# Kernel optimization log

Measured on AMD Instinct MI355X. Metric: run time of the kernel, lower is better.

## Reference

```python
import jax, jax.numpy as jnp
import numpy as np

jax.config.update("jax_enable_x64", True)

_FULL = 1 << 32
_MASK = _FULL - 1
_HALF = _FULL >> 1
_QUARTER = _HALF >> 1
_THREE_QUARTER = 3 * _QUARTER


def setup_inputs() -> dict:
    key = jax.random.key(0)
    num_symbols = 262144            # e.g. a 512x512 plane of {-1,+1} symbols
    num_bits = 2 * num_symbols      # compressed payload, ~2 bits/symbol budget
    payload_bits = jax.random.randint(key, (num_bits,), 0, 2, dtype=jnp.int64)
    return {
        "payload_bits": payload_bits,
        "total_freq": 4096,         # 1 << frequency_precision (12)
        "num_symbols": num_symbols,
        "context_bits": 8,
    }


def reference(payload_bits, total_freq, num_symbols, context_bits):
    bits = payload_bits.astype(jnp.int64)
    nb = bits.shape[0]
    num_states = 1 << context_bits
    smask = num_states - 1

    def read_bit(ptr):
        # _BitReader returns 0 past the end of the payload
        return jnp.where(ptr < nb, bits[jnp.clip(ptr, 0, nb - 1)], jnp.int64(0))

    # initial 32-bit code word
    idx32 = jnp.arange(32, dtype=jnp.int64)
    b32 = jnp.where(idx32 < nb, bits[jnp.clip(idx32, 0, nb - 1)], 0)
    code0 = jnp.sum(b32 << (31 - idx32))

    def renorm(carry):
        # E1/E2/E3 renormalization loop (bit-level, data dependent)
        def cond(c):
            low, high, code, ptr = c
            return (high < _HALF) | (low >= _HALF) | ((low >= _QUARTER) & (high < _THREE_QUARTER))

        def body(c):
            low, high, code, ptr = c
            sub = jnp.where(high < _HALF, jnp.int64(0),
                            jnp.where(low >= _HALF, jnp.int64(_HALF), jnp.int64(_QUARTER)))
            low = low - sub
            high = high - sub
            code = code - sub
            low = (low << 1) & _MASK
            high = ((high << 1) & _MASK) | 1
            code = ((code << 1) & _MASK) | read_bit(ptr)
            return (low, high, code, ptr + 1)

        return jax.lax.while_loop(cond, body, carry)

    def step(carry, _):
        low, high, code, ptr, state, count0, count1 = carry
        n0 = count0[state]
        n1 = count1[state]
        total = n0 + n1
        p0 = n0.astype(jnp.float64) / total.astype(jnp.float64)
        p0_freq = jnp.clip(jnp.rint(p0 * (total_freq - 2)) + 1.0, 1.0, float(total_freq - 1)).astype(jnp.int64)
        rng = high - low + 1                      # fits int64 (<= 2^32)
        scaled = ((code - low + 1) * total_freq - 1) // rng
        split = low + rng * p0_freq // total_freq
        bit = (scaled >= p0_freq).astype(jnp.int64)
        low2 = jnp.where(bit == 0, low, split)
        high2 = jnp.where(bit == 0, split - 1, high)
        low3, high3, code3, ptr3 = renorm((low2, high2, code, ptr))
        count0 = count0.at[state].add(1 - bit)
        count1 = count1.at[state].add(bit)
        state2 = ((state << 1) | bit) & smask
        return (low3, high3, code3, ptr3, state2, count0, count1), bit

    init = (
        jnp.int64(0),               # low
        jnp.int64(_MASK),           # high = 2^32 - 1
        code0.astype(jnp.int64),    # code
        jnp.int64(32),              # bit pointer (32 bits consumed)
        jnp.int64(0),               # context state
        jnp.ones(num_states, dtype=jnp.int64),  # count0 (Laplace init)
        jnp.ones(num_states, dtype=jnp.int64),  # count1
    )
    _, out_bits = jax.lax.scan(step, init, None, length=num_symbols)
    # map {0,1} -> {-1,+1} float32 symbols (reshape to bitstream.shape is metadata-only)
    return out_bits.astype(jnp.float32) * 2.0 - 1.0
```

## Files before the change

kernel.cpp:

```cpp
#include <hip/hip_runtime.h>


#define WORDS_LDS 16400
#define MAX_STATES 1024
#define OBITS_WORDS 8192

__device__ __forceinline__ long long ddiv_floor(long long n, long long d) {
    double qd = (double)n / (double)d;
    long long q = (long long)qd;
    long long r = n - q * d;
    q -= (r < 0);
    q += (r >= d);
    return q;
}

__device__ __forceinline__ void decode_fast(
    const unsigned* __restrict__ words, unsigned* tab, unsigned* obits,
    unsigned total_freq, int tf_shift, int num_symbols, int smask, unsigned pf0)
{
    const unsigned H = 0x80000000u;
    unsigned low = 0u, high = 0xFFFFFFFFu;
    unsigned dlt = words[0];
    unsigned long long bitbuf = (((unsigned long long)words[1]) << 32)
                              | (unsigned long long)words[2];
    int unavail = 64;
    unsigned pre = words[3];
    int widx = 4;
    unsigned wnext = words[4];

    const unsigned tfm2_2 = (total_freq - 2u) << 1;
    const double tfm2d = (double)(total_freq - 2u);
    const int tfm1 = (int)(total_freq - 1u);

    int st = 0, stP = -1;
    unsigned entN0 = 1u, entPK = 1u | (pf0 << 20);
    unsigned P0n0 = 1u, P0pk = entPK;
    unsigned P1n0 = 1u, P1pk = entPK;
    unsigned uN0p = 0u, uPKp = 0u;

    const int iters = num_symbols >> 5;
    for (int it = 0; it < iters; ++it) {
        unsigned obuf = 0u;
        #pragma unroll
        for (int u = 0; u < 32; ++u) {
            const int gbase = ((st << 2) & smask) * 2;
            const uint4 Ga = *reinterpret_cast<const uint4*>(tab + gbase);
            const uint4 Gb = *reinterpret_cast<const uint4*>(tab + gbase + 4);

            const unsigned pf  = entPK >> 20;
            const unsigned n1v = entPK & 0xFFFFFu;
            const unsigned n0v = entN0;
            const unsigned rngm1 = high - low;
            const unsigned long long P = (unsigned long long)pf * rngm1 + pf;
            const unsigned soff = (unsigned)(P >> tf_shift);
            const bool bt = (dlt >= soff);
            const unsigned bitv = bt ? 1u : 0u;
            const unsigned split = low + soff;
            low  = bt ? split : low;
            high = bt ? high : (split - 1u);
            dlt  = bt ? (dlt - soff) : dlt;
            obuf = (obuf << 1) | bitv;

            const unsigned nn0 = n0v + 1u - bitv;
            const unsigned nn1 = n1v + bitv;
            const unsigned tt  = nn0 + nn1;
            const unsigned d2  = tt << 1;
            const unsigned num2 = __umul24(tfm2_2, nn0) + tt;
            const float qf = (float)num2 * __builtin_amdgcn_rcpf((float)d2);
            unsigned qi = (unsigned)qf;
            int r = (int)(num2 - __umul24(qi, d2));
            if (r < 0)        { qi -= 1u; r += (int)d2; }
            if (r >= (int)d2) { qi += 1u; r -= (int)d2; }
            unsigned pfn = qi + 1u;
            if (__builtin_expect(__builtin_amdgcn_readfirstlane(r) == 0, 0)) {
                asm volatile("");
                double p0d = (double)(int)nn0 / (double)(int)tt;
                double pfd = rint(p0d * tfm2d) + 1.0;
                int pfi = (int)pfd;
                pfi = pfi < 1 ? 1 : (pfi > tfm1 ? tfm1 : pfi);
                pfn = (unsigned)pfi;
            }
            const unsigned npk = nn1 | (pfn << 20);

            const unsigned x = low ^ high;
            const int k = __builtin_clz(x);
            const unsigned aa   = ~(low << (k + 1));
            const unsigned bbv2 = (high << (k + 1)) | ((2u << k) - 1u);
            const int m = __builtin_clz(aa | bbv2);
            const int K = k + m;
            const unsigned sub  = (m != 0) ? H : 0u;
            const unsigned ones = (1u << K) - 1u;
            const unsigned tK = ((unsigned)(bitbuf >> 50)) >> (14 - K);
            low  = (low << K) - sub;
            high = (high << K) + ones - sub;
            dlt  = (dlt << K) | tK;
            bitbuf <<= K;
            unavail -= K;

            const bool need = (unavail <= 32);
            const unsigned long long ins =
                (((unsigned long long)pre) << 32) >> (unavail & 63);
            bitbuf |= need ? ins : 0ull;
            unavail += need ? 32 : 0;
            pre = need ? wnext : pre;
            widx += need ? 1 : 0;
            const int widxc = widx < (WORDS_LDS - 1) ? widx : (WORDS_LDS - 1);
            wnext = words[widxc];

            *reinterpret_cast<uint2*>(tab + 2 * st) = make_uint2(nn0, npk);

            const int stN = ((st << 1) | (int)bitv) & smask;
            unsigned en0 = bt ? P1n0 : P0n0;
            unsigned epk = bt ? P1pk : P0pk;
            if (__builtin_expect(stN == st || stN == stP, 0)) {
                asm volatile("");
                en0 = (stN == st) ? nn0 : uN0p;
                epk = (stN == st) ? npk : uPKp;
            }
            P0n0 = bt ? Gb.x : Ga.x;  P0pk = bt ? Gb.y : Ga.y;
            P1n0 = bt ? Gb.z : Ga.z;  P1pk = bt ? Gb.w : Ga.w;

            uN0p = nn0; uPKp = npk;
            stP = st; st = stN;
            entN0 = en0; entPK = epk;
        }
        obits[it] = obuf;
    }
}

__device__ void decode_serial_slow(
    const unsigned* __restrict__ words, unsigned* tab, unsigned* obits,
    const int* __restrict__ bits, int nb, int nwords,
    unsigned total_freq, int num_symbols, int smask,
    unsigned pf0, float* __restrict__ out)
{
    const unsigned H = 0x80000000u;
    unsigned low = 0u, high = 0xFFFFFFFFu;
    unsigned code = words[0];
    unsigned long long bitbuf = (((unsigned long long)words[1]) << 32) | (unsigned long long)words[2];
    int navail = 64;
    unsigned pre = words[3];
    int widx = 4;

    const double tfm2d = (double)(total_freq - 2u);
    const int tfm1 = (int)(total_freq - 1u);

    int state = 0;
    unsigned n0 = 1u, n1 = 1u, pf = pf0;
    int wIdx = 0;
    unsigned wN0 = 1u, wN1 = 1u, wPf = pf0;
    unsigned obuf = 0u;

    for (int s = 0; s < num_symbols; ++s) {
        const int c0 = (state << 1) & smask;
        uint4 q = *reinterpret_cast<const uint4*>(tab + 2 * c0);
        if (navail <= 32) {
            bitbuf |= ((unsigned long long)pre) << (32 - navail);
            navail += 32;
            unsigned nxt = 0u;
            if (widx < WORDS_LDS) nxt = words[widx];
            else if (widx < nwords) {
                unsigned g = 0u;
                long long base = ((long long)widx) << 5;
                for (int j = 0; j < 32; ++j) {
                    long long idx = base + j;
                    int b = (idx < (long long)nb) ? (bits[idx] & 1) : 0;
                    g |= ((unsigned)b) << (31 - j);
                }
                nxt = g;
            }
            pre = nxt;
            ++widx;
        }
        const unsigned rngm1 = high - low;
        const unsigned long long P = (unsigned long long)pf * rngm1 + pf;
        const unsigned soff = (unsigned)ddiv_floor((long long)P, (long long)total_freq);
        const unsigned dlt = code - low;
        const int bit = (dlt >= soff) ? 1 : 0;
        const unsigned split = low + soff;
        low  = bit ? split : low;
        high = bit ? high : (split - 1u);
        obuf = (obuf << 1) | (unsigned)bit;

        const unsigned nn0 = n0 + (unsigned)(1 - bit);
        const unsigned nn1 = n1 + (unsigned)bit;
        double p0d = (double)(int)nn0 / (double)(int)(nn0 + nn1);
        double pfd = rint(p0d * tfm2d) + 1.0;
        int pfi = (int)pfd;
        pfi = pfi < 1 ? 1 : (pfi > tfm1 ? tfm1 : pfi);
        unsigned pfn = (unsigned)pfi;

        const unsigned x = low ^ high;
        const int k = __builtin_clz(x);
        const unsigned aa = ~(low << (k + 1));
        const unsigned bbv = (high << (k + 1)) | ((2u << k) - 1u);
        const int m = __builtin_clz(aa | bbv);
        const int K = k + m;
        const unsigned sub = (m != 0) ? H : 0u;
        const unsigned ones = (1u << K) - 1u;
        const unsigned tE = (unsigned)(bitbuf >> 34);
        const unsigned tK = tE >> (30 - K);
        low  = (low << K) - sub;
        high = (high << K) + ones - sub;
        code = ((code << K) | tK) - sub;
        bitbuf <<= K;
        navail -= K;

        const int nidx = c0 | bit;
        const unsigned sw0 = bit ? q.z : q.x;
        const unsigned sw1 = bit ? q.w : q.y;
        const bool f2 = (nidx == wIdx);
        unsigned xn0 = f2 ? wN0 : sw0;
        unsigned xn1 = f2 ? wN1 : (sw1 & 0xFFFFFu);
        unsigned xpf = f2 ? wPf : (sw1 >> 20);
        *reinterpret_cast<uint2*>(tab + 2 * wIdx) = make_uint2(wN0, wN1 | (wPf << 20));
        wIdx = state; wN0 = nn0; wN1 = nn1; wPf = pfn;
        if (__builtin_expect(nidx == state, 0)) {
            asm volatile("");
            xn0 = nn0; xn1 = nn1; xpf = pfn;
        }
        state = nidx;
        n0 = xn0; n1 = xn1; pf = xpf;

        if ((s & 31) == 31) {
            int wo = s >> 5;
            if (wo < OBITS_WORDS) obits[wo] = obuf;
            else {
                int base = s & ~31;
                for (int j = 0; j < 32; ++j)
                    out[base + j] = ((obuf >> (31 - j)) & 1u) ? 1.0f : -1.0f;
            }
        }
    }
    if (num_symbols & 31) {
        int rem = num_symbols & 31;
        unsigned v = obuf << (32 - rem);
        int wo = num_symbols >> 5;
        if (wo < OBITS_WORDS) obits[wo] = v;
        else {
            int base = num_symbols & ~31;
            for (int j = 0; j < rem; ++j)
                out[base + j] = ((v >> (31 - j)) & 1u) ? 1.0f : -1.0f;
        }
    }
}

__global__ __launch_bounds__(256)
void EntropyDecoder_84928683311460_kernel(
    const int* __restrict__ bits,
    const int* __restrict__ tf_p,
    const int* __restrict__ ns_p,
    const int* __restrict__ cb_p,
    float* __restrict__ out,
    int nb)
{
    __shared__ unsigned words[WORDS_LDS];
    __shared__ __align__(16) unsigned tab[MAX_STATES * 2];
    __shared__ unsigned obits[OBITS_WORDS];

    const int tid = threadIdx.x;
    const unsigned total_freq = (unsigned)(*tf_p);
    const int num_symbols = *ns_p;
    const int context_bits = *cb_p;
    const int num_states = 1 << context_bits;
    const int smask = num_states - 1;
    const int nwords = (nb + 31) >> 5;

    for (int w = tid; w < WORDS_LDS; w += blockDim.x) {
        unsigned v = 0;
        int base = w << 5;
        if (base + 32 <= nb) {
            #pragma unroll
            for (int j = 0; j < 32; j += 4) {
                int4 b4 = *reinterpret_cast<const int4*>(bits + base + j);
                v |= ((unsigned)(b4.x & 1) << (31 - j))
                   | ((unsigned)(b4.y & 1) << (30 - j))
                   | ((unsigned)(b4.z & 1) << (29 - j))
                   | ((unsigned)(b4.w & 1) << (28 - j));
            }
        } else if (base < nb) {
            for (int j = 0; j < 32; ++j) {
                int idx = base + j;
                int b = (idx < nb) ? (bits[idx] & 1) : 0;
                v |= ((unsigned)b) << (31 - j);
            }
        }
        words[w] = v;
    }
    unsigned pf0;
    {
        double pfd = rint(0.5 * (double)(total_freq - 2u)) + 1.0;
        int t = (int)pfd;
        int tfm1 = (int)(total_freq - 1u);
        t = t < 1 ? 1 : (t > tfm1 ? tfm1 : t);
        pf0 = (unsigned)t;
    }
    for (int st = tid; st < num_states; st += blockDim.x) {
        tab[2 * st]     = 1u;
        tab[2 * st + 1] = 1u | (pf0 << 20);
    }
    __syncthreads();

    const int tf_shift = 31 - __builtin_clz(total_freq);
    const bool pow2 = (total_freq & (total_freq - 1u)) == 0u;
    const unsigned long long bound =
        2ull * (unsigned long long)(total_freq - 2u) * (unsigned long long)(num_symbols + 1)
        + (unsigned long long)(num_symbols + 2);
    const bool fast = pow2 && total_freq >= 8u && total_freq <= 4096u
                      && bound < (1ull << 31)
                      && num_states >= 4 && num_states <= 256
                      && (num_symbols & 31) == 0
                      && num_symbols <= OBITS_WORDS * 32
                      && nwords <= 16384;

    if (fast) {
        if (tid == 0) {
            decode_fast(words, tab, obits, total_freq, tf_shift,
                        num_symbols, smask, pf0);
        }
    } else {
        if (tid == 0) {
            decode_serial_slow(words, tab, obits, bits, nb, nwords, total_freq,
                               num_symbols, smask, pf0, out);
        }
    }
    __syncthreads();

    const int nwout = (num_symbols + 31) >> 5;
    const int npk = nwout < OBITS_WORDS ? nwout : OBITS_WORDS;
    for (int w = tid; w < npk; w += blockDim.x) {
        unsigned v = obits[w];
        int base = w << 5;
        if (base + 32 <= num_symbols) {
            #pragma unroll
            for (int j = 0; j < 32; j += 4) {
                float4 o;
                o.x = ((v >> (31 - j)) & 1u) ? 1.0f : -1.0f;
                o.y = ((v >> (30 - j)) & 1u) ? 1.0f : -1.0f;
                o.z = ((v >> (29 - j)) & 1u) ? 1.0f : -1.0f;
                o.w = ((v >> (28 - j)) & 1u) ? 1.0f : -1.0f;
                *reinterpret_cast<float4*>(out + base + j) = o;
            }
        } else {
            for (int j = 0; j < 32 && base + j < num_symbols; ++j)
                out[base + j] = ((v >> (31 - j)) & 1u) ? 1.0f : -1.0f;
        }
    }
}

extern "C" void kernel_launch(void* const* d_in, const int* in_sizes, int n_in,
                              void* d_out, int out_size, void* d_ws, size_t ws_size,
                              hipStream_t stream) {
    const int* bits = (const int*)d_in[0];
    const int* tf   = (const int*)d_in[1];
    const int* ns   = (const int*)d_in[2];
    const int* cb   = (const int*)d_in[3];
    float* out = (float*)d_out;
    int nb = in_sizes[0];

    hipLaunchKernelGGL(EntropyDecoder_84928683311460_kernel,
                       dim3(1), dim3(256), 0, stream,
                       bits, tf, ns, cb, out, nb);
}
```

Baseline: 84.91 ms.

## Decode two symbols per iteration with speculative probability updates

Restructures the serial arithmetic decoder loop so each iteration handles two symbols. The next-state table entries for both possible child states and grandchild states are prefetched from LDS one step ahead. Both possible probability updates (bit 0 and bit 1) are computed before the bit is known, so the division work runs alongside the range comparison. The goal is to shorten the loop-carried dependency chain of a single-thread decoder. In exchange there is more speculative arithmetic per symbol and more complex forwarding logic for state aliasing, which risks correctness bugs. The bitstream refill now happens once per two symbols, which relies on two renormalizations never consuming more than the buffered bits.

```diff
diff --git a/kernel.cpp b/kernel.cpp
--- a/kernel.cpp
+++ b/kernel.cpp
@@ -32,99 +32,194 @@
     const double tfm2d = (double)(total_freq - 2u);
     const int tfm1 = (int)(total_freq - 1u);
 
-    int st = 0, stP = -1;
-    unsigned entN0 = 1u, entPK = 1u | (pf0 << 20);
-    unsigned P0n0 = 1u, P0pk = entPK;
-    unsigned P1n0 = 1u, P1pk = entPK;
-    unsigned uN0p = 0u, uPKp = 0u;
-
-    const int iters = num_symbols >> 5;
+    int st = 0;
+    unsigned eN0 = 1u, ePK = 1u | (pf0 << 20);
+    int u1pS = -1; unsigned u1pN0 = 0u, u1pPK = 0u;
+
+    int cb = (st << 1) & smask;
+    int gb = (st << 2) & smask;
+    uint4 C  = *reinterpret_cast<const uint4*>(tab + 2 * cb);
+    uint4 Ga = *reinterpret_cast<const uint4*>(tab + 2 * gb);
+    uint4 Gb = *reinterpret_cast<const uint4*>(tab + 2 * gb + 4);
+
+    const int iters = num_symbols >> 1;
+    unsigned obuf = 0u;
     for (int it = 0; it < iters; ++it) {
-        unsigned obuf = 0u;
-        #pragma unroll
-        for (int u = 0; u < 32; ++u) {
-            const int gbase = ((st << 2) & smask) * 2;
-            const uint4 Ga = *reinterpret_cast<const uint4*>(tab + gbase);
-            const uint4 Gb = *reinterpret_cast<const uint4*>(tab + gbase + 4);
-
-            const unsigned pf  = entPK >> 20;
-            const unsigned n1v = entPK & 0xFFFFFu;
-            const unsigned n0v = entN0;
-            const unsigned rngm1 = high - low;
-            const unsigned long long P = (unsigned long long)pf * rngm1 + pf;
-            const unsigned soff = (unsigned)(P >> tf_shift);
-            const bool bt = (dlt >= soff);
-            const unsigned bitv = bt ? 1u : 0u;
-            const unsigned split = low + soff;
-            low  = bt ? split : low;
-            high = bt ? high : (split - 1u);
-            dlt  = bt ? (dlt - soff) : dlt;
-            obuf = (obuf << 1) | bitv;
-
-            const unsigned nn0 = n0v + 1u - bitv;
-            const unsigned nn1 = n1v + bitv;
-            const unsigned tt  = nn0 + nn1;
-            const unsigned d2  = tt << 1;
-            const unsigned num2 = __umul24(tfm2_2, nn0) + tt;
-            const float qf = (float)num2 * __builtin_amdgcn_rcpf((float)d2);
-            unsigned qi = (unsigned)qf;
-            int r = (int)(num2 - __umul24(qi, d2));
-            if (r < 0)        { qi -= 1u; r += (int)d2; }
-            if (r >= (int)d2) { qi += 1u; r -= (int)d2; }
-            unsigned pfn = qi + 1u;
-            if (__builtin_expect(__builtin_amdgcn_readfirstlane(r) == 0, 0)) {
-                asm volatile("");
-                double p0d = (double)(int)nn0 / (double)(int)tt;
-                double pfd = rint(p0d * tfm2d) + 1.0;
-                int pfi = (int)pfd;
-                pfi = pfi < 1 ? 1 : (pfi > tfm1 ? tfm1 : pfi);
-                pfn = (unsigned)pfi;
-            }
-            const unsigned npk = nn1 | (pfn << 20);
-
-            const unsigned x = low ^ high;
+        const unsigned pf1 = ePK >> 20;
+        const unsigned n1a = ePK & 0xFFFFFu;
+        const unsigned n0a = eN0;
+        const unsigned rngm1 = high - low;
+        const unsigned long long P1 = (unsigned long long)pf1 * rngm1 + pf1;
+        const unsigned soff1 = (unsigned)(P1 >> tf_shift);
+        const bool bt1 = (dlt >= soff1);
+        const unsigned b1 = bt1 ? 1u : 0u;
+        const unsigned split1 = low + soff1;
+        unsigned lo = bt1 ? split1 : low;
+        unsigned hi = bt1 ? high   : (split1 - 1u);
+        unsigned dl = bt1 ? (dlt - soff1) : dlt;
+
+        const unsigned tt1 = n0a + n1a + 1u;
+        const unsigned d21 = tt1 << 1;
+        const float rcp1 = __builtin_amdgcn_rcpf((float)d21);
+        const unsigned nA0 = n0a + 1u;
+        const unsigned numA = __umul24(tfm2_2, nA0) + tt1;
+        const unsigned numB = numA - tfm2_2;
+        unsigned qA = (unsigned)((float)numA * rcp1);
+        unsigned qB = (unsigned)((float)numB * rcp1);
+        int rA = (int)(numA - __umul24(qA, d21));
+        if (rA < 0)         { qA -= 1u; rA += (int)d21; }
+        if (rA >= (int)d21) { qA += 1u; rA -= (int)d21; }
+        int rB = (int)(numB - __umul24(qB, d21));
+        if (rB < 0)         { qB -= 1u; rB += (int)d21; }
+        if (rB >= (int)d21) { qB += 1u; rB -= (int)d21; }
+        const unsigned nn0_1 = bt1 ? n0a : nA0;
+        const unsigned nn1_1 = bt1 ? (n1a + 1u) : n1a;
+        unsigned pfn1 = (bt1 ? qB : qA) + 1u;
+        const int r1 = bt1 ? rB : rA;
+        if (__builtin_expect(r1 == 0, 0)) {
+            asm volatile("");
+            double p0d = (double)(int)nn0_1 / (double)(int)tt1;
+            double pfd = rint(p0d * tfm2d) + 1.0;
+            int pfi = (int)pfd;
+            pfi = pfi < 1 ? 1 : (pfi > tfm1 ? tfm1 : pfi);
+            pfn1 = (unsigned)pfi;
+        }
+        const unsigned npk1 = nn1_1 | (pfn1 << 20);
+
+        {
+            const unsigned x = lo ^ hi;
             const int k = __builtin_clz(x);
-            const unsigned aa   = ~(low << (k + 1));
-            const unsigned bbv2 = (high << (k + 1)) | ((2u << k) - 1u);
-            const int m = __builtin_clz(aa | bbv2);
+            const unsigned aa = ~(lo << (k + 1));
+            const unsigned bv = (hi << (k + 1)) | ((2u << k) - 1u);
+            const int m = __builtin_clz(aa | bv);
             const int K = k + m;
-            const unsigned sub  = (m != 0) ? H : 0u;
+            const unsigned sub = (m != 0) ? H : 0u;
             const unsigned ones = (1u << K) - 1u;
             const unsigned tK = ((unsigned)(bitbuf >> 50)) >> (14 - K);
-            low  = (low << K) - sub;
-            high = (high << K) + ones - sub;
-            dlt  = (dlt << K) | tK;
+            lo = (lo << K) - sub;
+            hi = (hi << K) + ones - sub;
+            dl = (dl << K) | tK;
             bitbuf <<= K;
             unavail -= K;
-
-            const bool need = (unavail <= 32);
-            const unsigned long long ins =
-                (((unsigned long long)pre) << 32) >> (unavail & 63);
-            bitbuf |= need ? ins : 0ull;
-            unavail += need ? 32 : 0;
-            pre = need ? wnext : pre;
-            widx += need ? 1 : 0;
-            const int widxc = widx < (WORDS_LDS - 1) ? widx : (WORDS_LDS - 1);
-            wnext = words[widxc];
-
-            *reinterpret_cast<uint2*>(tab + 2 * st) = make_uint2(nn0, npk);
-
-            const int stN = ((st << 1) | (int)bitv) & smask;
-            unsigned en0 = bt ? P1n0 : P0n0;
-            unsigned epk = bt ? P1pk : P0pk;
-            if (__builtin_expect(stN == st || stN == stP, 0)) {
-                asm volatile("");
-                en0 = (stN == st) ? nn0 : uN0p;
-                epk = (stN == st) ? npk : uPKp;
-            }
-            P0n0 = bt ? Gb.x : Ga.x;  P0pk = bt ? Gb.y : Ga.y;
-            P1n0 = bt ? Gb.z : Ga.z;  P1pk = bt ? Gb.w : Ga.w;
-
-            uN0p = nn0; uPKp = npk;
-            stP = st; st = stN;
-            entN0 = en0; entPK = epk;
-        }
-        obits[it] = obuf;
+        }
+
+        const int s1 = cb | (int)b1;
+        unsigned e2N0 = bt1 ? C.z : C.x;
+        unsigned e2PK = bt1 ? C.w : C.y;
+        if (__builtin_expect(s1 == u1pS, 0)) {
+            asm volatile("");
+            e2N0 = u1pN0; e2PK = u1pPK;
+        }
+        {
+            const bool sl = (s1 == st);
+            e2N0 = sl ? nn0_1 : e2N0;
+            e2PK = sl ? npk1  : e2PK;
+        }
+        const unsigned pf2 = e2PK >> 20;
+        const unsigned n1b = e2PK & 0xFFFFFu;
+        const unsigned n0b = e2N0;
+        const unsigned rngm2 = hi - lo;
+        const unsigned long long P2 = (unsigned long long)pf2 * rngm2 + pf2;
+        const unsigned soff2 = (unsigned)(P2 >> tf_shift);
+        const bool bt2 = (dl >= soff2);
+        const unsigned b2 = bt2 ? 1u : 0u;
+        const unsigned split2 = lo + soff2;
+        unsigned lo2 = bt2 ? split2 : lo;
+        unsigned hi2 = bt2 ? hi     : (split2 - 1u);
+        unsigned dl2 = bt2 ? (dl - soff2) : dl;
+
+        const unsigned tt2 = n0b + n1b + 1u;
+        const unsigned d22 = tt2 << 1;
+        const float rcp2 = __builtin_amdgcn_rcpf((float)d22);
+        const unsigned nC0 = n0b + 1u;
+        const unsigned numC = __umul24(tfm2_2, nC0) + tt2;
+        const unsigned numD = numC - tfm2_2;
+        unsigned qC = (unsigned)((float)numC * rcp2);
+        unsigned qD = (unsigned)((float)numD * rcp2);
+        int rC = (int)(numC - __umul24(qC, d22));
+        if (rC < 0)         { qC -= 1u; rC += (int)d22; }
+        if (rC >= (int)d22) { qC += 1u; rC -= (int)d22; }
+        int rD = (int)(numD - __umul24(qD, d22));
+        if (rD < 0)         { qD -= 1u; rD += (int)d22; }
+        if (rD >= (int)d22) { qD += 1u; rD -= (int)d22; }
+        const unsigned nn0_2 = bt2 ? n0b : nC0;
+        const unsigned nn1_2 = bt2 ? (n1b + 1u) : n1b;
+        unsigned pfn2 = (bt2 ? qD : qC) + 1u;
+        const int r2 = bt2 ? rD : rC;
+        if (__builtin_expect(r2 == 0, 0)) {
+            asm volatile("");
+            double p0d = (double)(int)nn0_2 / (double)(int)tt2;
+            double pfd = rint(p0d * tfm2d) + 1.0;
+            int pfi = (int)pfd;
+            pfi = pfi < 1 ? 1 : (pfi > tfm1 ? tfm1 : pfi);
+            pfn2 = (unsigned)pfi;
+        }
+        const unsigned npk2 = nn1_2 | (pfn2 << 20);
+
+        int K2;
+        {
+            const unsigned x = lo2 ^ hi2;
+            const int k = __builtin_clz(x);
+            const unsigned aa = ~(lo2 << (k + 1));
+            const unsigned bv = (hi2 << (k + 1)) | ((2u << k) - 1u);
+            const int m = __builtin_clz(aa | bv);
+            K2 = k + m;
+            const unsigned sub = (m != 0) ? H : 0u;
+            const unsigned ones = (1u << K2) - 1u;
+            const unsigned tK = ((unsigned)(bitbuf >> 50)) >> (14 - K2);
+            lo2 = (lo2 << K2) - sub;
+            hi2 = (hi2 << K2) + ones - sub;
+            dl2 = (dl2 << K2) | tK;
+            bitbuf <<= K2;
+            unavail -= K2;
+        }
+
+        const int s2 = ((s1 << 1) | (int)b2) & smask;
+        const unsigned t0N = bt2 ? Ga.z : Ga.x;
+        const unsigned t0P = bt2 ? Ga.w : Ga.y;
+        const unsigned t1N = bt2 ? Gb.z : Gb.x;
+        const unsigned t1P = bt2 ? Gb.w : Gb.y;
+        unsigned eN = bt1 ? t1N : t0N;
+        unsigned eP = bt1 ? t1P : t0P;
+        if (__builtin_expect(s2 == u1pS, 0)) {
+            asm volatile("");
+            eN = u1pN0; eP = u1pPK;
+        }
+        {
+            const bool c = (s2 == st);
+            eN = c ? nn0_1 : eN;
+            eP = c ? npk1  : eP;
+        }
+        if (__builtin_expect(s2 == s1, 0)) {
+            asm volatile("");
+            eN = nn0_2; eP = npk2;
+        }
+
+        *reinterpret_cast<uint2*>(tab + 2 * st) = make_uint2(nn0_1, npk1);
+        const int cbN = (s2 << 1) & smask;
+        const int gbN = (s2 << 2) & smask;
+        const uint4 Cn  = *reinterpret_cast<const uint4*>(tab + 2 * cbN);
+        const uint4 GaN = *reinterpret_cast<const uint4*>(tab + 2 * gbN);
+        const uint4 GbN = *reinterpret_cast<const uint4*>(tab + 2 * gbN + 4);
+        *reinterpret_cast<uint2*>(tab + 2 * s1) = make_uint2(nn0_2, npk2);
+
+        u1pS = s1; u1pN0 = nn0_2; u1pPK = npk2;
+        st = s2; eN0 = eN; ePK = eP;
+        cb = cbN; gb = gbN; C = Cn; Ga = GaN; Gb = GbN;
+        low = lo2; high = hi2; dlt = dl2;
+
+        obuf = (obuf << 2) | (b1 << 1) | b2;
+        const bool need = (unavail <= 32);
+        const unsigned long long ins =
+            (((unsigned long long)pre) << 32) >> (unavail & 63);
+        bitbuf |= need ? ins : 0ull;
+        unavail += need ? 32 : 0;
+        pre = need ? wnext : pre;
+        widx += need ? 1 : 0;
+        const int wc = widx < (WORDS_LDS - 1) ? widx : (WORDS_LDS - 1);
+        wnext = words[wc];
+
+        if ((it & 15) == 15) obits[it >> 4] = obuf;
     }
 }
 
@@ -309,17 +404,15 @@
     const bool fast = pow2 && total_freq >= 8u && total_freq <= 4096u
                       && bound < (1ull << 31)
                       && num_states >= 4 && num_states <= 256
-                      && (num_symbols & 31) == 0
+                      && (num_symbols & 31) == 0 && num_symbols > 0
                       && num_symbols <= OBITS_WORDS * 32
                       && nwords <= 16384;
 
-    if (fast) {
-        if (tid == 0) {
+    if (tid == 0) {
+        if (fast) {
             decode_fast(words, tab, obits, total_freq, tf_shift,
                         num_symbols, smask, pf0);
-        }
-    } else {
-        if (tid == 0) {
+        } else {
             decode_serial_slow(words, tab, obits, bits, nb, nwords, total_freq,
                                num_symbols, smask, pf0, out);
         }
```

After: 85.04 ms. Within noise of the previous version (+0.2%).
